# Performance work log

Hardware: AMD Instinct MI355X
Metric: run time of the kernel (lower is better)

## Reference

```python
import jax, jax.numpy as jnp
import numpy as np

N_NODES = 100000


def gcn_conv(x, src, dst, w, W, b, n):
    """PyG GCNConv: out = D^{-1/2} (A+I) D^{-1/2} (x @ W) + b (self-loops weight 1)."""
    loop = jnp.arange(n, dtype=src.dtype)
    s = jnp.concatenate([src, loop])
    d = jnp.concatenate([dst, loop])
    ew = jnp.concatenate([w, jnp.ones((n,), x.dtype)])
    deg = jax.ops.segment_sum(ew, d, num_segments=n)            # degree of target nodes
    dinv = jnp.where(deg > 0, jax.lax.rsqrt(deg), jnp.zeros_like(deg))
    norm = dinv[s] * ew * dinv[d]                               # [E+N]
    h = x @ W                                                   # [N, out] dense transform first
    msg = h[s] * norm[:, None]                                  # gather + scale
    out = jax.ops.segment_sum(msg, d, num_segments=n)           # scatter-add aggregate
    return out + b


def setup_inputs() -> dict:
    key = jax.random.key(0)
    k1, k2, k3, k4, k5, k6 = jax.random.split(key, 6)
    in_dim, hid, out_dim = 128, 128, 64
    n_edges = 1600000
    x = jax.random.normal(k1, (N_NODES, in_dim), dtype=jnp.float32)
    edge_index = jax.random.randint(k2, (2, n_edges), 0, N_NODES, dtype=jnp.int32)
    edge_weight = jax.random.uniform(k3, (n_edges,), dtype=jnp.float32)
    # Glorot-style weights, zero bias (as in GCNConv defaults)
    W1 = jax.random.normal(k4, (in_dim, hid), dtype=jnp.float32) / np.sqrt(in_dim)
    b1 = jnp.zeros((hid,), jnp.float32)
    W2 = jax.random.normal(k5, (hid, out_dim), dtype=jnp.float32) / np.sqrt(hid)
    b2 = jnp.zeros((out_dim,), jnp.float32)
    return {"x": x, "edge_index": edge_index, "edge_weight": edge_weight,
            "W1": W1, "b1": b1, "W2": W2, "b2": b2}


def reference(x, edge_index, edge_weight, W1, b1, W2, b2):
    src, dst = edge_index[0], edge_index[1]
    h = gcn_conv(x, src, dst, edge_weight, W1, b1, N_NODES)
    h = jax.nn.relu(h)
    # dropout is identity in eval mode
    out = gcn_conv(h, src, dst, edge_weight, W2, b2, N_NODES)
    return out
```

## Files before the change

kernel.cpp:

```cpp
#include <hip/hip_runtime.h>
#include <cstdint>
#include <cstddef>


typedef unsigned long long u64;
typedef unsigned int u32;
typedef unsigned short u16;
typedef __attribute__((ext_vector_type(8))) short bf16x8;
typedef __attribute__((ext_vector_type(4))) float f32x4;

__device__ __forceinline__ float bflo(u32 u) { return __uint_as_float(u << 16); }
__device__ __forceinline__ float bfhi(u32 u) { return __uint_as_float(u & 0xffff0000u); }
__device__ __forceinline__ u32 f2bf(float f) {
  u32 u = __float_as_uint(f);
  return (u + 0x7fffu + ((u >> 16) & 1u)) >> 16;
}
__device__ __forceinline__ u32 pack2bf(float lo, float hi) {
  return f2bf(lo) | (f2bf(hi) << 16);
}
__device__ __forceinline__ float dec_norm(u32 rec) {
  return (float)(rec & 32767u) * 3.0517578125e-05f;
}

__global__ void degrank_kernel(const int* __restrict__ dst, const float* __restrict__ w,
                               u64* packed, u16* __restrict__ rank, int E) {
  int e = blockIdx.x * 256 + threadIdx.x;
  if (e < E) {
    int d = dst[e];
    u64 add = (1ull << 48) | (u64)(w[e] * 4294967296.0f);
    u64 old = atomicAdd(&packed[d], add);
    rank[e] = (u16)(old >> 48);
  }
}

__global__ __launch_bounds__(256) void gemm1_kernel(const float* __restrict__ x,
                                                    const float* __restrict__ W1,
                                                    u16* __restrict__ h1, int M) {
  __shared__ u16 Wt[128][136];
  const int tid = threadIdx.x;
  for (int i = tid; i < 128 * 128; i += 256) {
    int c = i >> 7, k = i & 127;
    Wt[c][k] = (u16)f2bf(W1[(size_t)k * 128 + c]);
  }
  __syncthreads();

  const int wv = tid >> 6;
  const int l = tid & 63;
  const int c16 = l & 15;
  const int kg = l >> 4;
  const int arow = blockIdx.x * 64 + wv * 16 + c16;
  const bool rok = arow < M;

  bf16x8 ahi[4], alo[4];
  #pragma unroll
  for (int kk = 0; kk < 4; ++kk) {
    float v[8];
    if (rok) {
      float4 p0 = *reinterpret_cast<const float4*>(x + (size_t)arow * 128 + kk * 32 + kg * 8);
      float4 p1 = *reinterpret_cast<const float4*>(x + (size_t)arow * 128 + kk * 32 + kg * 8 + 4);
      v[0] = p0.x; v[1] = p0.y; v[2] = p0.z; v[3] = p0.w;
      v[4] = p1.x; v[5] = p1.y; v[6] = p1.z; v[7] = p1.w;
    } else {
      #pragma unroll
      for (int j = 0; j < 8; ++j) v[j] = 0.f;
    }
    #pragma unroll
    for (int j = 0; j < 8; ++j) {
      u32 hb = f2bf(v[j]);
      float hf = __uint_as_float(hb << 16);
      u32 lb = f2bf(v[j] - hf);
      ahi[kk][j] = (short)hb;
      alo[kk][j] = (short)lb;
    }
  }

  #pragma unroll
  for (int ct = 0; ct < 8; ++ct) {
    f32x4 acc = {0.f, 0.f, 0.f, 0.f};
    #pragma unroll
    for (int kk = 0; kk < 4; ++kk) {
      bf16x8 b = *reinterpret_cast<const bf16x8*>(&Wt[ct * 16 + c16][kk * 32 + kg * 8]);
      acc = __builtin_amdgcn_mfma_f32_16x16x32_bf16(alo[kk], b, acc, 0, 0, 0);
      acc = __builtin_amdgcn_mfma_f32_16x16x32_bf16(ahi[kk], b, acc, 0, 0, 0);
    }
    #pragma unroll
    for (int r = 0; r < 4; ++r) {
      int gr = blockIdx.x * 64 + wv * 16 + kg * 4 + r;
      if (gr < M) h1[(size_t)gr * 128 + ct * 16 + c16] = (u16)f2bf(acc[r]);
    }
  }
}

__global__ void scan_kernel(const u64* __restrict__ packed, int* __restrict__ rowstart,
                            int* __restrict__ bsum, int* __restrict__ boff,
                            u32* __restrict__ counter, float* __restrict__ dinvp,
                            int n, int nblk) {
  __shared__ int wsum[4];
  __shared__ bool amLast;
  int b = blockIdx.x;
  int base = b * 1024;
  int tid = threadIdx.x;
  int lane = tid & 63, wv = tid >> 6;
  int idx = base + tid * 4;
  int v0 = 0, v1 = 0, v2 = 0, v3 = 0;
  #pragma unroll
  for (int j = 0; j < 4; ++j) {
    if (idx + j < n) {
      u64 p = packed[idx + j];
      int c = (int)(p >> 48);
      if (j == 0) v0 = c; else if (j == 1) v1 = c; else if (j == 2) v2 = c; else v3 = c;
      float deg = 1.0f + (float)((double)(p & 0xFFFFFFFFFFFFull) * 2.3283064365386963e-10);
      dinvp[idx + j] = rsqrtf(deg);
    }
  }
  int tsum = v0 + v1 + v2 + v3;
  int inc = tsum;
  #pragma unroll
  for (int off = 1; off < 64; off <<= 1) {
    int u = __shfl_up(inc, off, 64);
    if (lane >= off) inc += u;
  }
  if (lane == 63) wsum[wv] = inc;
  __syncthreads();
  int woff = 0;
  for (int w2 = 0; w2 < wv; ++w2) woff += wsum[w2];
  int texc = woff + inc - tsum;
  if (idx     < n) rowstart[idx]     = texc;
  if (idx + 1 < n) rowstart[idx + 1] = texc + v0;
  if (idx + 2 < n) rowstart[idx + 2] = texc + v0 + v1;
  if (idx + 3 < n) rowstart[idx + 3] = texc + v0 + v1 + v2;
  if (tid == 255) {
    bsum[b] = woff + inc;
    if (b == nblk - 1) rowstart[n] = woff + inc;
  }
  __threadfence();
  if (tid == 0) amLast = (atomicAdd(counter, 1u) == (u32)(nblk - 1));
  __syncthreads();
  if (amLast) {
    __threadfence();
    int v = (tid < nblk) ? bsum[tid] : 0;
    int inc2 = v;
    #pragma unroll
    for (int off = 1; off < 64; off <<= 1) {
      int u = __shfl_up(inc2, off, 64);
      if (lane >= off) inc2 += u;
    }
    if (lane == 63) wsum[wv] = inc2;
    __syncthreads();
    int woff2 = 0;
    for (int w2 = 0; w2 < wv; ++w2) woff2 += wsum[w2];
    if (tid < nblk) boff[tid] = woff2 + inc2 - v;
  }
}

__global__ void fill_kernel(const int* __restrict__ src, const int* __restrict__ dst,
                            const float* __restrict__ w, const u16* __restrict__ rank,
                            const float* __restrict__ dinv, const int* __restrict__ rowstart,
                            const int* __restrict__ boff, u32* __restrict__ erec, int E) {
  int e = blockIdx.x * 256 + threadIdx.x;
  if (e < E) {
    int s = src[e], d = dst[e];
    int pos = rowstart[d] + boff[d >> 10] + (int)rank[e];
    float nrm = dinv[s] * w[e] * dinv[d];
    u32 q = (u32)(nrm * 32768.0f);
    if (q > 32767u) q = 32767u;
    erec[pos] = ((u32)s << 15) | q;
  }
}

__global__ __launch_bounds__(512) void agg1_gemm2_kernel(
    const uint2* __restrict__ H2, const int* __restrict__ rowstart,
    const int* __restrict__ boff, const u32* __restrict__ erec,
    const float* __restrict__ dinv, const float* __restrict__ b1,
    const float* __restrict__ W2, u16* __restrict__ h2, int n) {
  __shared__ u16 A1[64][136];
  __shared__ u16 Wt[64][136];
  const int tid = threadIdx.x;
  const int wave = tid >> 6;
  const int lane = tid & 63;
  const int base = blockIdx.x * 64;

  for (int i = tid; i < 64 * 128; i += 512) {
    int c = i >> 7, k = i & 127;
    Wt[c][k] = (u16)f2bf(W2[(size_t)k * 64 + c]);
  }

  const int hl = lane & 31;
  #pragma unroll
  for (int p = 0; p < 4; ++p) {
    int r = wave * 8 + p * 2 + (lane >> 5);
    int node = base + r;
    if (node < n) {
      float dv = dinv[node];
      float ns = dv * dv;
      uint2 hv = H2[(size_t)node * 32 + hl];
      float a0 = ns * bflo(hv.x), a1v = ns * bfhi(hv.x);
      float a2 = ns * bflo(hv.y), a3 = ns * bfhi(hv.y);
      int e  = rowstart[node] + boff[node >> 10];
      int e1 = rowstart[node + 1] + boff[(node + 1) >> 10];
      for (; e + 3 < e1; e += 4) {
        u32 r0 = erec[e], r1 = erec[e + 1], r2 = erec[e + 2], r3 = erec[e + 3];
        uint2 v0 = H2[(size_t)(r0 >> 15) * 32 + hl];
        uint2 v1 = H2[(size_t)(r1 >> 15) * 32 + hl];
        uint2 v2 = H2[(size_t)(r2 >> 15) * 32 + hl];
        uint2 v3 = H2[(size_t)(r3 >> 15) * 32 + hl];
        float w0 = dec_norm(r0), w1 = dec_norm(r1), w2 = dec_norm(r2), w3 = dec_norm(r3);
        a0  += w0 * bflo(v0.x) + w1 * bflo(v1.x) + w2 * bflo(v2.x) + w3 * bflo(v3.x);
        a1v += w0 * bfhi(v0.x) + w1 * bfhi(v1.x) + w2 * bfhi(v2.x) + w3 * bfhi(v3.x);
        a2  += w0 * bflo(v0.y) + w1 * bflo(v1.y) + w2 * bflo(v2.y) + w3 * bflo(v3.y);
        a3  += w0 * bfhi(v0.y) + w1 * bfhi(v1.y) + w2 * bfhi(v2.y) + w3 * bfhi(v3.y);
      }
      for (; e < e1; ++e) {
        u32 rr = erec[e];
        uint2 v = H2[(size_t)(rr >> 15) * 32 + hl];
        float w = dec_norm(rr);
        a0 += w * bflo(v.x); a1v += w * bfhi(v.x);
        a2 += w * bflo(v.y); a3  += w * bfhi(v.y);
      }
      float4 bb = reinterpret_cast<const float4*>(b1)[hl];
      a0  = fmaxf(a0 + bb.x, 0.f);
      a1v = fmaxf(a1v + bb.y, 0.f);
      a2  = fmaxf(a2 + bb.z, 0.f);
      a3  = fmaxf(a3 + bb.w, 0.f);
      *reinterpret_cast<uint2*>(&A1[r][hl * 4]) =
          make_uint2(pack2bf(a0, a1v), pack2bf(a2, a3));
    } else {
      *reinterpret_cast<uint2*>(&A1[r][hl * 4]) = make_uint2(0u, 0u);
    }
  }
  __syncthreads();

  const int c16 = lane & 15;
  const int kg = lane >> 4;
  #pragma unroll
  for (int t = wave * 2; t < wave * 2 + 2; ++t) {
    int rt = t >> 2;
    int ctile = t & 3;
    f32x4 acc = {0.f, 0.f, 0.f, 0.f};
    #pragma unroll
    for (int kk = 0; kk < 4; ++kk) {
      bf16x8 a = *reinterpret_cast<const bf16x8*>(&A1[rt * 16 + c16][kk * 32 + kg * 8]);
      bf16x8 b = *reinterpret_cast<const bf16x8*>(&Wt[ctile * 16 + c16][kk * 32 + kg * 8]);
      acc = __builtin_amdgcn_mfma_f32_16x16x32_bf16(a, b, acc, 0, 0, 0);
    }
    #pragma unroll
    for (int r = 0; r < 4; ++r) {
      int grow = base + rt * 16 + kg * 4 + r;
      if (grow < n) h2[(size_t)grow * 64 + ctile * 16 + c16] = (u16)f2bf(acc[r]);
    }
  }
}

__global__ __launch_bounds__(256) void agg64_kernel(
    const u32* __restrict__ H, const int* __restrict__ rowstart,
    const int* __restrict__ boff, const u32* __restrict__ erec,
    const float* __restrict__ dinv, const float* __restrict__ bias,
    float2* __restrict__ out2, int n) {
  int wid = (blockIdx.x * 256 + threadIdx.x) >> 6;
  int lane = threadIdx.x & 63;
  int node = wid * 2 + (lane >> 5);
  int hl = lane & 31;
  if (node >= n) return;
  float dv = dinv[node];
  float ns = dv * dv;
  u32 hv = H[(size_t)node * 32 + hl];
  float a0 = ns * bflo(hv), a1 = ns * bfhi(hv);
  int e  = rowstart[node] + boff[node >> 10];
  int e1 = rowstart[node + 1] + boff[(node + 1) >> 10];
  for (; e + 3 < e1; e += 4) {
    u32 r0 = erec[e], r1 = erec[e + 1], r2 = erec[e + 2], r3 = erec[e + 3];
    u32 v0 = H[(size_t)(r0 >> 15) * 32 + hl];
    u32 v1 = H[(size_t)(r1 >> 15) * 32 + hl];
    u32 v2 = H[(size_t)(r2 >> 15) * 32 + hl];
    u32 v3 = H[(size_t)(r3 >> 15) * 32 + hl];
    float w0 = dec_norm(r0), w1 = dec_norm(r1), w2 = dec_norm(r2), w3 = dec_norm(r3);
    a0 += w0 * bflo(v0) + w1 * bflo(v1) + w2 * bflo(v2) + w3 * bflo(v3);
    a1 += w0 * bfhi(v0) + w1 * bfhi(v1) + w2 * bfhi(v2) + w3 * bfhi(v3);
  }
  for (; e < e1; ++e) {
    u32 rr = erec[e];
    u32 v = H[(size_t)(rr >> 15) * 32 + hl];
    float w = dec_norm(rr);
    a0 += w * bflo(v);
    a1 += w * bfhi(v);
  }
  float2 bb = reinterpret_cast<const float2*>(bias)[hl];
  out2[(size_t)node * 32 + hl] = make_float2(a0 + bb.x, a1 + bb.y);
}

extern "C" void kernel_launch(void* const* d_in, const int* in_sizes, int n_in,
                              void* d_out, int out_size, void* d_ws, size_t ws_size,
                              hipStream_t stream) {
  const float* x  = (const float*)d_in[0];
  const int*   ei = (const int*)d_in[1];
  const float* ew = (const float*)d_in[2];
  const float* W1 = (const float*)d_in[3];
  const float* b1 = (const float*)d_in[4];
  const float* W2 = (const float*)d_in[5];
  const float* b2 = (const float*)d_in[6];
  float* out = (float*)d_out;
  const int N = in_sizes[0] / 128;
  const int E = in_sizes[2];
  const int* src = ei;
  const int* dst = ei + E;

  char* wsB = (char*)d_ws;
  size_t off = 0;
  auto alloc = [&](size_t bytes) {
    void* p = wsB + off;
    off += ((bytes + 255) / 256) * 256;
    return p;
  };
  u64*   packed  = (u64*)alloc((size_t)N * 8);
  u32*   counter = (u32*)alloc(256);
  float* dinv    = (float*)alloc((size_t)N * 4);
  u16*   rank    = (u16*)alloc((size_t)E * 2);
  int*   rowst   = (int*)alloc((size_t)(N + 1) * 4);
  int*   bsum    = (int*)alloc(256 * 4);
  int*   boff    = (int*)alloc(256 * 4);
  u32*   erec    = (u32*)alloc((size_t)E * 4);
  u16*   h1      = (u16*)alloc((size_t)N * 128 * 2);
  u16*   h2      = (u16*)alloc((size_t)N * 64 * 2);

  const int eb = (E + 255) / 256;
  const int nbx = (N + 63) / 64;
  const int nblk = (N + 1023) / 1024;

  hipMemsetAsync(d_ws, 0, (size_t)N * 8 + 256, stream);
  degrank_kernel<<<eb, 256, 0, stream>>>(dst, ew, packed, rank, E);
  gemm1_kernel<<<nbx, 256, 0, stream>>>(x, W1, h1, N);
  scan_kernel<<<nblk, 256, 0, stream>>>(packed, rowst, bsum, boff, counter, dinv, N, nblk);
  fill_kernel<<<eb, 256, 0, stream>>>(src, dst, ew, rank, dinv, rowst, boff, erec, E);

  agg1_gemm2_kernel<<<nbx, 512, 0, stream>>>((const uint2*)h1, rowst, boff, erec, dinv,
                                             b1, W2, h2, N);
  const int ab = (N + 7) / 8;
  agg64_kernel<<<ab, 256, 0, stream>>>((const u32*)h2, rowst, boff, erec, dinv, b2,
                                       (float2*)out, N);
}
```

Baseline: 431.7 us.

## Fold symmetric degree normalization into node features instead of per-edge weights

Stores only the raw edge weight in each edge record and applies D^{-1/2} on the source side by pre-scaling rows of h1/h2 in the GEMM epilogues, then on the destination side once per node after aggregation. This removes two random dinv gathers per edge from the fill kernel and the self-loop dinv² term. To get dinv, gemm1 now has to run after the scan kernel. Quantizing the raw weight instead of the full norm changes precision, and values of 1 or more are still clamped to 32767.

```diff
diff --git a/kernel.cpp b/kernel.cpp
--- a/kernel.cpp
+++ b/kernel.cpp
@@ -18,7 +18,7 @@
 __device__ __forceinline__ u32 pack2bf(float lo, float hi) {
   return f2bf(lo) | (f2bf(hi) << 16);
 }
-__device__ __forceinline__ float dec_norm(u32 rec) {
+__device__ __forceinline__ float dec_w(u32 rec) {
   return (float)(rec & 32767u) * 3.0517578125e-05f;
 }
 
@@ -30,64 +30,6 @@
     u64 add = (1ull << 48) | (u64)(w[e] * 4294967296.0f);
     u64 old = atomicAdd(&packed[d], add);
     rank[e] = (u16)(old >> 48);
-  }
-}
-
-__global__ __launch_bounds__(256) void gemm1_kernel(const float* __restrict__ x,
-                                                    const float* __restrict__ W1,
-                                                    u16* __restrict__ h1, int M) {
-  __shared__ u16 Wt[128][136];
-  const int tid = threadIdx.x;
-  for (int i = tid; i < 128 * 128; i += 256) {
-    int c = i >> 7, k = i & 127;
-    Wt[c][k] = (u16)f2bf(W1[(size_t)k * 128 + c]);
-  }
-  __syncthreads();
-
-  const int wv = tid >> 6;
-  const int l = tid & 63;
-  const int c16 = l & 15;
-  const int kg = l >> 4;
-  const int arow = blockIdx.x * 64 + wv * 16 + c16;
-  const bool rok = arow < M;
-
-  bf16x8 ahi[4], alo[4];
-  #pragma unroll
-  for (int kk = 0; kk < 4; ++kk) {
-    float v[8];
-    if (rok) {
-      float4 p0 = *reinterpret_cast<const float4*>(x + (size_t)arow * 128 + kk * 32 + kg * 8);
-      float4 p1 = *reinterpret_cast<const float4*>(x + (size_t)arow * 128 + kk * 32 + kg * 8 + 4);
-      v[0] = p0.x; v[1] = p0.y; v[2] = p0.z; v[3] = p0.w;
-      v[4] = p1.x; v[5] = p1.y; v[6] = p1.z; v[7] = p1.w;
-    } else {
-      #pragma unroll
-      for (int j = 0; j < 8; ++j) v[j] = 0.f;
-    }
-    #pragma unroll
-    for (int j = 0; j < 8; ++j) {
-      u32 hb = f2bf(v[j]);
-      float hf = __uint_as_float(hb << 16);
-      u32 lb = f2bf(v[j] - hf);
-      ahi[kk][j] = (short)hb;
-      alo[kk][j] = (short)lb;
-    }
-  }
-
-  #pragma unroll
-  for (int ct = 0; ct < 8; ++ct) {
-    f32x4 acc = {0.f, 0.f, 0.f, 0.f};
-    #pragma unroll
-    for (int kk = 0; kk < 4; ++kk) {
-      bf16x8 b = *reinterpret_cast<const bf16x8*>(&Wt[ct * 16 + c16][kk * 32 + kg * 8]);
-      acc = __builtin_amdgcn_mfma_f32_16x16x32_bf16(alo[kk], b, acc, 0, 0, 0);
-      acc = __builtin_amdgcn_mfma_f32_16x16x32_bf16(ahi[kk], b, acc, 0, 0, 0);
-    }
-    #pragma unroll
-    for (int r = 0; r < 4; ++r) {
-      int gr = blockIdx.x * 64 + wv * 16 + kg * 4 + r;
-      if (gr < M) h1[(size_t)gr * 128 + ct * 16 + c16] = (u16)f2bf(acc[r]);
-    }
   }
 }
 
@@ -153,18 +95,83 @@
   }
 }
 
+__global__ __launch_bounds__(256) void gemm1_kernel(const float* __restrict__ x,
+                                                    const float* __restrict__ W1,
+                                                    const float* __restrict__ dinv,
+                                                    u16* __restrict__ h1, int M) {
+  __shared__ u16 Wt[128][136];
+  const int tid = threadIdx.x;
+  for (int i = tid; i < 128 * 128; i += 256) {
+    int c = i >> 7, k = i & 127;
+    Wt[c][k] = (u16)f2bf(W1[(size_t)k * 128 + c]);
+  }
+  __syncthreads();
+
+  const int wv = tid >> 6;
+  const int l = tid & 63;
+  const int c16 = l & 15;
+  const int kg = l >> 4;
+  const int arow = blockIdx.x * 64 + wv * 16 + c16;
+  const bool rok = arow < M;
+
+  bf16x8 ahi[4], alo[4];
+  #pragma unroll
+  for (int kk = 0; kk < 4; ++kk) {
+    float v[8];
+    if (rok) {
+      float4 p0 = *reinterpret_cast<const float4*>(x + (size_t)arow * 128 + kk * 32 + kg * 8);
+      float4 p1 = *reinterpret_cast<const float4*>(x + (size_t)arow * 128 + kk * 32 + kg * 8 + 4);
+      v[0] = p0.x; v[1] = p0.y; v[2] = p0.z; v[3] = p0.w;
+      v[4] = p1.x; v[5] = p1.y; v[6] = p1.z; v[7] = p1.w;
+    } else {
+      #pragma unroll
+      for (int j = 0; j < 8; ++j) v[j] = 0.f;
+    }
+    #pragma unroll
+    for (int j = 0; j < 8; ++j) {
+      u32 hb = f2bf(v[j]);
+      float hf = __uint_as_float(hb << 16);
+      u32 lb = f2bf(v[j] - hf);
+      ahi[kk][j] = (short)hb;
+      alo[kk][j] = (short)lb;
+    }
+  }
+
+  float dvv[4];
+  #pragma unroll
+  for (int r = 0; r < 4; ++r) {
+    int gr = blockIdx.x * 64 + wv * 16 + kg * 4 + r;
+    dvv[r] = (gr < M) ? dinv[gr] : 0.f;
+  }
+
+  #pragma unroll
+  for (int ct = 0; ct < 8; ++ct) {
+    f32x4 acc = {0.f, 0.f, 0.f, 0.f};
+    #pragma unroll
+    for (int kk = 0; kk < 4; ++kk) {
+      bf16x8 b = *reinterpret_cast<const bf16x8*>(&Wt[ct * 16 + c16][kk * 32 + kg * 8]);
+      acc = __builtin_amdgcn_mfma_f32_16x16x32_bf16(alo[kk], b, acc, 0, 0, 0);
+      acc = __builtin_amdgcn_mfma_f32_16x16x32_bf16(ahi[kk], b, acc, 0, 0, 0);
+    }
+    #pragma unroll
+    for (int r = 0; r < 4; ++r) {
+      int gr = blockIdx.x * 64 + wv * 16 + kg * 4 + r;
+      if (gr < M) h1[(size_t)gr * 128 + ct * 16 + c16] = (u16)f2bf(dvv[r] * acc[r]);
+    }
+  }
+}
+
 __global__ void fill_kernel(const int* __restrict__ src, const int* __restrict__ dst,
                             const float* __restrict__ w, const u16* __restrict__ rank,
-                            const float* __restrict__ dinv, const int* __restrict__ rowstart,
-                            const int* __restrict__ boff, u32* __restrict__ erec, int E) {
+                            const int* __restrict__ rowstart, const int* __restrict__ boff,
+                            u32* __restrict__ erec, int E) {
   int e = blockIdx.x * 256 + threadIdx.x;
   if (e < E) {
-    int s = src[e], d = dst[e];
+    int d = dst[e];
     int pos = rowstart[d] + boff[d >> 10] + (int)rank[e];
-    float nrm = dinv[s] * w[e] * dinv[d];
-    u32 q = (u32)(nrm * 32768.0f);
+    u32 q = (u32)(w[e] * 32768.0f);
     if (q > 32767u) q = 32767u;
-    erec[pos] = ((u32)s << 15) | q;
+    erec[pos] = ((u32)src[e] << 15) | q;
   }
 }
 
@@ -192,10 +199,9 @@
     int node = base + r;
     if (node < n) {
       float dv = dinv[node];
-      float ns = dv * dv;
       uint2 hv = H2[(size_t)node * 32 + hl];
-      float a0 = ns * bflo(hv.x), a1v = ns * bfhi(hv.x);
-      float a2 = ns * bflo(hv.y), a3 = ns * bfhi(hv.y);
+      float a0 = bflo(hv.x), a1v = bfhi(hv.x);
+      float a2 = bflo(hv.y), a3 = bfhi(hv.y);
       int e  = rowstart[node] + boff[node >> 10];
       int e1 = rowstart[node + 1] + boff[(node + 1) >> 10];
       for (; e + 3 < e1; e += 4) {
@@ -204,7 +210,7 @@
         uint2 v1 = H2[(size_t)(r1 >> 15) * 32 + hl];
         uint2 v2 = H2[(size_t)(r2 >> 15) * 32 + hl];
         uint2 v3 = H2[(size_t)(r3 >> 15) * 32 + hl];
-        float w0 = dec_norm(r0), w1 = dec_norm(r1), w2 = dec_norm(r2), w3 = dec_norm(r3);
+        float w0 = dec_w(r0), w1 = dec_w(r1), w2 = dec_w(r2), w3 = dec_w(r3);
         a0  += w0 * bflo(v0.x) + w1 * bflo(v1.x) + w2 * bflo(v2.x) + w3 * bflo(v3.x);
         a1v += w0 * bfhi(v0.x) + w1 * bfhi(v1.x) + w2 * bfhi(v2.x) + w3 * bfhi(v3.x);
         a2  += w0 * bflo(v0.y) + w1 * bflo(v1.y) + w2 * bflo(v2.y) + w3 * bflo(v3.y);
@@ -213,15 +219,15 @@
       for (; e < e1; ++e) {
         u32 rr = erec[e];
         uint2 v = H2[(size_t)(rr >> 15) * 32 + hl];
-        float w = dec_norm(rr);
+        float w = dec_w(rr);
         a0 += w * bflo(v.x); a1v += w * bfhi(v.x);
         a2 += w * bflo(v.y); a3  += w * bfhi(v.y);
       }
       float4 bb = reinterpret_cast<const float4*>(b1)[hl];
-      a0  = fmaxf(a0 + bb.x, 0.f);
-      a1v = fmaxf(a1v + bb.y, 0.f);
-      a2  = fmaxf(a2 + bb.z, 0.f);
-      a3  = fmaxf(a3 + bb.w, 0.f);
+      a0  = fmaxf(dv * a0 + bb.x, 0.f);
+      a1v = fmaxf(dv * a1v + bb.y, 0.f);
+      a2  = fmaxf(dv * a2 + bb.z, 0.f);
+      a3  = fmaxf(dv * a3 + bb.w, 0.f);
       *reinterpret_cast<uint2*>(&A1[r][hl * 4]) =
           make_uint2(pack2bf(a0, a1v), pack2bf(a2, a3));
     } else {
@@ -246,7 +252,10 @@
     #pragma unroll
     for (int r = 0; r < 4; ++r) {
       int grow = base + rt * 16 + kg * 4 + r;
-      if (grow < n) h2[(size_t)grow * 64 + ctile * 16 + c16] = (u16)f2bf(acc[r]);
+      if (grow < n) {
+        float dv2 = dinv[grow];
+        h2[(size_t)grow * 64 + ctile * 16 + c16] = (u16)f2bf(dv2 * acc[r]);
+      }
     }
   }
 }
@@ -262,9 +271,8 @@
   int hl = lane & 31;
   if (node >= n) return;
   float dv = dinv[node];
-  float ns = dv * dv;
   u32 hv = H[(size_t)node * 32 + hl];
-  float a0 = ns * bflo(hv), a1 = ns * bfhi(hv);
+  float a0 = bflo(hv), a1 = bfhi(hv);
   int e  = rowstart[node] + boff[node >> 10];
   int e1 = rowstart[node + 1] + boff[(node + 1) >> 10];
   for (; e + 3 < e1; e += 4) {
@@ -273,19 +281,19 @@
     u32 v1 = H[(size_t)(r1 >> 15) * 32 + hl];
     u32 v2 = H[(size_t)(r2 >> 15) * 32 + hl];
     u32 v3 = H[(size_t)(r3 >> 15) * 32 + hl];
-    float w0 = dec_norm(r0), w1 = dec_norm(r1), w2 = dec_norm(r2), w3 = dec_norm(r3);
+    float w0 = dec_w(r0), w1 = dec_w(r1), w2 = dec_w(r2), w3 = dec_w(r3);
     a0 += w0 * bflo(v0) + w1 * bflo(v1) + w2 * bflo(v2) + w3 * bflo(v3);
     a1 += w0 * bfhi(v0) + w1 * bfhi(v1) + w2 * bfhi(v2) + w3 * bfhi(v3);
   }
   for (; e < e1; ++e) {
     u32 rr = erec[e];
     u32 v = H[(size_t)(rr >> 15) * 32 + hl];
-    float w = dec_norm(rr);
+    float w = dec_w(rr);
     a0 += w * bflo(v);
     a1 += w * bfhi(v);
   }
   float2 bb = reinterpret_cast<const float2*>(bias)[hl];
-  out2[(size_t)node * 32 + hl] = make_float2(a0 + bb.x, a1 + bb.y);
+  out2[(size_t)node * 32 + hl] = make_float2(dv * a0 + bb.x, dv * a1 + bb.y);
 }
 
 extern "C" void kernel_launch(void* const* d_in, const int* in_sizes, int n_in,
@@ -328,9 +336,9 @@
 
   hipMemsetAsync(d_ws, 0, (size_t)N * 8 + 256, stream);
   degrank_kernel<<<eb, 256, 0, stream>>>(dst, ew, packed, rank, E);
-  gemm1_kernel<<<nbx, 256, 0, stream>>>(x, W1, h1, N);
   scan_kernel<<<nblk, 256, 0, stream>>>(packed, rowst, bsum, boff, counter, dinv, N, nblk);
-  fill_kernel<<<eb, 256, 0, stream>>>(src, dst, ew, rank, dinv, rowst, boff, erec, E);
+  gemm1_kernel<<<nbx, 256, 0, stream>>>(x, W1, dinv, h1, N);
+  fill_kernel<<<eb, 256, 0, stream>>>(src, dst, ew, rank, rowst, boff, erec, E);
 
   agg1_gemm2_kernel<<<nbx, 512, 0, stream>>>((const uint2*)h1, rowst, boff, erec, dinv,
                                              b1, W2, h2, N);
```

Measured after the change: 418.5 us. 3.0% less time.
